# Kernel tuning notes

Hardware: AMD Instinct MI355X
Metric: run time of the kernel (lower is better)

The kernel has to match this reference:

```python
import jax, jax.numpy as jnp
import numpy as np

C = 256
RED = 8
DQK = C // RED  # 32


def setup_inputs() -> dict:
    key = jax.random.key(0)
    ks = jax.random.split(key, 8)
    B, H, W = 8, 64, 64
    x = jax.random.normal(ks[0], (B, C, H, W), dtype=jnp.float32)
    # 1x1 conv weights stored as [out, in]; biases [out]
    Wq = jax.random.normal(ks[1], (DQK, C), dtype=jnp.float32) * 0.02
    bq = jax.random.normal(ks[2], (DQK,), dtype=jnp.float32) * 0.02
    Wk = jax.random.normal(ks[3], (DQK, C), dtype=jnp.float32) * 0.02
    bk = jax.random.normal(ks[4], (DQK,), dtype=jnp.float32) * 0.02
    Wv = jax.random.normal(ks[5], (C, C), dtype=jnp.float32) * 0.02
    bv = jax.random.normal(ks[6], (C,), dtype=jnp.float32) * 0.02
    gamma = jax.random.normal(ks[7], (1,), dtype=jnp.float32) * 0.1
    return {"x": x, "Wq": Wq, "bq": bq, "Wk": Wk, "bk": bk, "Wv": Wv, "bv": bv, "gamma": gamma}


def reference(x, Wq, bq, Wk, bk, Wv, bv, gamma):
    B, Cc, H, W = x.shape
    N = H * W
    xf = x.reshape(B, Cc, N)                       # (B, C, N)
    # 1x1 convs == per-pixel dense projections
    q = jnp.einsum('dc,bcn->bdn', Wq, xf) + bq[None, :, None]   # (B, d, N)
    k = jnp.einsum('dc,bcn->bdn', Wk, xf) + bk[None, :, None]   # (B, d, N)
    v = jnp.einsum('ec,bcn->ben', Wv, xf) + bv[None, :, None]   # (B, C, N)
    # energy[b,i,j] = q[b,:,i] . k[b,:,j]; softmax over j (no scaling, SAGAN-style)
    energy = jnp.einsum('bdi,bdj->bij', q, k)      # (B, N, N)
    attn = jax.nn.softmax(energy, axis=-1)
    # out[b,c,i] = sum_j v[b,c,j] * attn[b,i,j]
    out = jnp.einsum('bcj,bij->bci', v, attn)      # (B, C, N)
    out = out.reshape(B, Cc, H, W)
    return gamma[0] * out + x
```

## Files before the change

kernel.cpp:

```cpp
#include <hip/hip_runtime.h>

#define NB 8
#define CCH 256
#define DQK 32
#define NPIX 4096

typedef __attribute__((ext_vector_type(8))) short short8;
typedef __attribute__((ext_vector_type(4))) float f32x4;
typedef __attribute__((ext_vector_type(4))) unsigned short ushort4v;

static __device__ __forceinline__ unsigned short f2bf(float f) {
  unsigned int u = __builtin_bit_cast(unsigned int, f);
  u += 0x7FFFu + ((u >> 16) & 1u);
  return (unsigned short)(u >> 16);
}
static __device__ __forceinline__ unsigned int pack2bf(float a, float b) {
  return (unsigned int)f2bf(a) | ((unsigned int)f2bf(b) << 16);
}

__global__ __launch_bounds__(256) void wconv_kernel(
    const float* __restrict__ Wq, const float* __restrict__ Wk,
    const float* __restrict__ Wv, unsigned short* __restrict__ Wbf) {
  const int e = (blockIdx.x * 256 + threadIdx.x) * 4;
  const int m = e >> 8, c = e & 255;
  const float* src;
  if (m < 32) src = Wq + (size_t)m * CCH;
  else if (m < 64) src = Wk + (size_t)(m - 32) * CCH;
  else src = Wv + (size_t)(m - 64) * CCH;
  const float4 v = *(const float4*)(src + c);
  ushort4v o;
  o[0] = f2bf(v.x); o[1] = f2bf(v.y); o[2] = f2bf(v.z); o[3] = f2bf(v.w);
  *(ushort4v*)(Wbf + e) = o;
}

__global__ __launch_bounds__(256) void xt_kernel(
    const float* __restrict__ x, unsigned short* __restrict__ xT) {
  const int t = threadIdx.x;
  const int b = blockIdx.x & 7;
  const int p = (blockIdx.x >> 3) * 64 + (t & 63);
  const int w = t >> 6;
  const float* xb = x + (size_t)b * CCH * NPIX + p;
  unsigned short* dst = xT + ((size_t)b * NPIX + p) * CCH + 64 * w;
#pragma unroll
  for (int g = 0; g < 8; ++g) {
    short8 o;
#pragma unroll
    for (int j = 0; j < 8; ++j)
      o[j] = (short)f2bf(xb[(size_t)(64 * w + 8 * g + j) * NPIX]);
    *(short8*)(dst + 8 * g) = o;
  }
}

__global__ __launch_bounds__(256) void proj_kernel(
    const unsigned short* __restrict__ xT, const unsigned short* __restrict__ Wbf,
    const float* __restrict__ bq, const float* __restrict__ bk,
    const float* __restrict__ bv,
    unsigned short* __restrict__ Qb, unsigned short* __restrict__ Kb,
    unsigned short* __restrict__ Vb) {
  const int t = threadIdx.x;
  const int b = blockIdx.x & 7;
  const int i0 = (blockIdx.x >> 3) * 64;
  const int w = t >> 6, l = t & 63;
  const int lc = l & 15, lg = l >> 4;
  const int m0w = 80 * w;
  const unsigned short* xrow = xT + ((size_t)b * NPIX + i0 + lc) * CCH + lg * 8;
  const unsigned short* wrow = Wbf + (size_t)(m0w + lc) * CCH + lg * 8;

  f32x4 acc[5][4];
#pragma unroll
  for (int mt = 0; mt < 5; ++mt)
#pragma unroll
    for (int nt = 0; nt < 4; ++nt) acc[mt][nt] = (f32x4){0.f, 0.f, 0.f, 0.f};

#pragma unroll
  for (int kk = 0; kk < 8; ++kk) {
    short8 af[5];
#pragma unroll
    for (int mt = 0; mt < 5; ++mt)
      af[mt] = *(const short8*)(wrow + (size_t)(mt * 16) * CCH + kk * 32);
    short8 bf[4];
#pragma unroll
    for (int nt = 0; nt < 4; ++nt)
      bf[nt] = *(const short8*)(xrow + (size_t)(nt * 16) * CCH + kk * 32);
#pragma unroll
    for (int nt = 0; nt < 4; ++nt)
#pragma unroll
      for (int mt = 0; mt < 5; ++mt)
        acc[mt][nt] = __builtin_amdgcn_mfma_f32_16x16x32_bf16(af[mt], bf[nt], acc[mt][nt], 0, 0, 0);
  }
#pragma unroll
  for (int mt = 0; mt < 5; ++mt) {
    const int mbase = m0w + mt * 16;
    const int mrow = mbase + 4 * lg;
    if (mbase < 64) {
      const bool isQ = (mbase < 32);
      const float scale = isQ ? 1.44269504f : 1.0f;
      const float* bias = isQ ? (bq + mrow) : (bk + (mrow - 32));
      unsigned short* dst = isQ ? (Qb + (size_t)b * NPIX * DQK + mrow)
                                : (Kb + (size_t)b * NPIX * DQK + (mrow - 32));
      const float b0 = bias[0], b1 = bias[1], b2 = bias[2], b3 = bias[3];
#pragma unroll
      for (int nt = 0; nt < 4; ++nt) {
        const int i = i0 + nt * 16 + lc;
        ushort4v o;
        o[0] = f2bf((acc[mt][nt][0] + b0) * scale);
        o[1] = f2bf((acc[mt][nt][1] + b1) * scale);
        o[2] = f2bf((acc[mt][nt][2] + b2) * scale);
        o[3] = f2bf((acc[mt][nt][3] + b3) * scale);
        *(ushort4v*)(dst + (size_t)i * DQK) = o;
      }
    } else {
      const int vrow = mbase - 64 + 4 * lg;
#pragma unroll
      for (int jj = 0; jj < 4; ++jj) {
        const float bias = bv[vrow + jj];
        unsigned short* vdst = Vb + ((size_t)b * CCH + vrow + jj) * NPIX + i0;
#pragma unroll
        for (int nt = 0; nt < 4; ++nt)
          vdst[nt * 16 + lc] = f2bf(acc[mt][nt][jj] + bias);
      }
    }
  }
}

union AttnSmem {
  unsigned short p[2][64 * 64];
  float tsc[4][16 * 68];
};

__global__ __launch_bounds__(256, 2) void attn_kernel(
    const unsigned short* __restrict__ Qb,
    const unsigned short* __restrict__ Kb,
    const unsigned short* __restrict__ Vb,
    const float* __restrict__ x,
    const float* __restrict__ gammap,
    float* __restrict__ out) {
  __shared__ AttnSmem sm;
  __shared__ float l_lds[64];
  const int t = threadIdx.x;
  const int w = t >> 6, l = t & 63;
  const int lc = l & 15, lg = l >> 4;
  const int b = blockIdx.x & 7;
  const int q0 = (blockIdx.x >> 3) * 64;

  const unsigned short* Kl = Kb + (size_t)b * NPIX * DQK + (size_t)lc * DQK + lg * 8;
  const unsigned short* Vl = Vb + ((size_t)b * CCH + 64 * w + lc) * NPIX + lg * 8;
  const short8 qa = *(const short8*)(Qb + (size_t)b * NPIX * DQK +
                                     (size_t)(q0 + 16 * w + lc) * DQK + lg * 8);
  const f32x4 zero4 = {0.f, 0.f, 0.f, 0.f};
  const int pwb = (16 * w + lc) * 128;
  const int psw = (lc & 7) << 3;

  f32x4 acc[4][4];
#pragma unroll
  for (int mt = 0; mt < 4; ++mt)
#pragma unroll
    for (int ct = 0; ct < 4; ++ct) acc[mt][ct] = (f32x4){0.f, 0.f, 0.f, 0.f};
  float psum = 0.f;

  short8 vfA[8], vfB[8], kfA[4], kfB[4];

#pragma unroll
  for (int kt = 0; kt < 4; ++kt)
    kfA[kt] = *(const short8*)(Kl + (size_t)(kt * 16) * DQK);
#pragma unroll
  for (int kt = 0; kt < 4; ++kt) {
    const f32x4 s = __builtin_amdgcn_mfma_f32_16x16x32_bf16(kfA[kt], qa, zero4, 0, 0, 0);
    const float p0 = __builtin_exp2f(s[0]), p1 = __builtin_exp2f(s[1]);
    const float p2 = __builtin_exp2f(s[2]), p3 = __builtin_exp2f(s[3]);
    psum += (p0 + p1) + (p2 + p3);
    uint2 wv; wv.x = pack2bf(p0, p1); wv.y = pack2bf(p2, p3);
    *(uint2*)((char*)sm.p[0] + pwb + (((16 * kt + 4 * lg) ^ psw) << 1)) = wv;
  }
#pragma unroll
  for (int ct = 0; ct < 4; ++ct) {
    vfA[ct] = *(const short8*)(Vl + (size_t)(16 * ct) * NPIX);
    vfA[4 + ct] = *(const short8*)(Vl + (size_t)(16 * ct) * NPIX + 32);
  }
#pragma unroll
  for (int kt = 0; kt < 4; ++kt)
    kfB[kt] = *(const short8*)(Kl + (size_t)(64 + kt * 16) * DQK);
  __syncthreads();

#define ATTN_ITER(T, BUF, VF, KF_CUR, VF_NXT, KF_NXT)                               \
  {                                                                                 \
    const int t_ = (T);                                                             \
    if (t_ < 63) {      \
      const size_t kb2 = (size_t)(t_ + 1) * 64;                                     \
      _Pragma("unroll") for (int ct = 0; ct < 4; ++ct) {                            \
        VF_NXT[ct] = *(const short8*)(Vl + (size_t)(16 * ct) * NPIX + kb2);         \
        VF_NXT[4 + ct] = *(const short8*)(Vl + (size_t)(16 * ct) * NPIX + kb2 + 32);\
      }                                                                             \
      if (t_ < 62) {                                                                \
        const size_t kk2 = (size_t)(t_ + 2) * 64;                                   \
        _Pragma("unroll") for (int kt = 0; kt < 4; ++kt)                            \
          KF_NXT[kt] = *(const short8*)(Kl + (kk2 + kt * 16) * DQK);                \
      }                                                                             \
    }                                                                               \
    unsigned short* pb_ = sm.p[BUF];                                                \
    unsigned short* pb2_ = sm.p[(BUF) ^ 1];                                         \
    _Pragma("unroll") for (int ks2 = 0; ks2 < 2; ++ks2) {                           \
      short8 pa[4];                                                                 \
      _Pragma("unroll") for (int mt = 0; mt < 4; ++mt)                              \
        pa[mt] = *(const short8*)((const char*)pb_ + (16 * mt + lc) * 128 +         \
                                  (((32 * ks2 + 8 * lg) ^ psw) << 1));              \
      _Pragma("unroll") for (int ct = 0; ct < 4; ++ct)                              \
        _Pragma("unroll") for (int mt = 0; mt < 4; ++mt)                            \
          acc[mt][ct] = __builtin_amdgcn_mfma_f32_16x16x32_bf16(                    \
              pa[mt], VF[ks2 * 4 + ct], acc[mt][ct], 0, 0, 0);                      \
    }                                                                               \
    if (t_ < 63) {                                                                  \
      _Pragma("unroll") for (int kt = 0; kt < 4; ++kt) {                            \
        const f32x4 s = __builtin_amdgcn_mfma_f32_16x16x32_bf16(                    \
            KF_CUR[kt], qa, zero4, 0, 0, 0);                                        \
        const float p0 = __builtin_exp2f(s[0]), p1 = __builtin_exp2f(s[1]);         \
        const float p2 = __builtin_exp2f(s[2]), p3 = __builtin_exp2f(s[3]);         \
        psum += (p0 + p1) + (p2 + p3);                                              \
        uint2 wv; wv.x = pack2bf(p0, p1); wv.y = pack2bf(p2, p3);                   \
        *(uint2*)((char*)pb2_ + pwb + (((16 * kt + 4 * lg) ^ psw) << 1)) = wv;      \
      }                                                                             \
    }                                                                               \
    asm volatile("s_waitcnt lgkmcnt(0)\n\ts_barrier" ::: "memory");                 \
  }

  for (int ks = 0; ks < 64; ks += 2) {
    ATTN_ITER(ks, 0, vfA, kfB, vfB, kfA);
    ATTN_ITER(ks + 1, 1, vfB, kfA, vfA, kfB);
  }
#undef ATTN_ITER

  {
    float v = psum;
    v += __shfl_xor(v, 16);
    v += __shfl_xor(v, 32);
    if (l < 16) l_lds[16 * w + lc] = v;
  }
  __syncthreads();

  const float g = gammap[0];
  float linv4[4][4];
#pragma unroll
  for (int mt = 0; mt < 4; ++mt)
#pragma unroll
    for (int jj = 0; jj < 4; ++jj)
      linv4[mt][jj] = g / l_lds[16 * mt + 4 * lg + jj];

  float* tw = sm.tsc[w];
  const float* xbp = x + (size_t)b * CCH * NPIX;
  float* ob = out + (size_t)b * CCH * NPIX;
#pragma unroll
  for (int ct = 0; ct < 4; ++ct) {
#pragma unroll
    for (int mt = 0; mt < 4; ++mt) {
      f32x4 o;
#pragma unroll
      for (int jj = 0; jj < 4; ++jj) o[jj] = acc[mt][ct][jj] * linv4[mt][jj];
      *(f32x4*)(tw + lc * 68 + 16 * mt + 4 * lg) = o;
    }
#pragma unroll
    for (int r = 0; r < 4; ++r) {
      const int crow = 4 * r + lg;
      const f32x4 o = *(const f32x4*)(tw + crow * 68 + lc * 4);
      const size_t idx = (size_t)(64 * w + 16 * ct + crow) * NPIX + (size_t)(q0 + lc * 4);
      const float4 xv = *(const float4*)(xbp + idx);
      float4 ov;
      ov.x = o[0] + xv.x; ov.y = o[1] + xv.y; ov.z = o[2] + xv.z; ov.w = o[3] + xv.w;
      *(float4*)(ob + idx) = ov;
    }
  }
}

extern "C" void kernel_launch(void* const* d_in, const int* in_sizes, int n_in,
                              void* d_out, int out_size, void* d_ws, size_t ws_size,
                              hipStream_t stream) {
  (void)in_sizes; (void)n_in; (void)out_size; (void)ws_size;
  const float* x     = (const float*)d_in[0];
  const float* Wq    = (const float*)d_in[1];
  const float* bq    = (const float*)d_in[2];
  const float* Wk    = (const float*)d_in[3];
  const float* bk    = (const float*)d_in[4];
  const float* Wv    = (const float*)d_in[5];
  const float* bv    = (const float*)d_in[6];
  const float* gamma = (const float*)d_in[7];

  unsigned short* Wbf = (unsigned short*)d_ws;
  unsigned short* Qb  = Wbf + 320 * CCH;
  unsigned short* Kb  = Qb + (size_t)NB * NPIX * DQK;
  unsigned short* Vb  = Kb + (size_t)NB * NPIX * DQK;
  unsigned short* xT  = (unsigned short*)d_out;

  wconv_kernel<<<80, 256, 0, stream>>>(Wq, Wk, Wv, Wbf);
  xt_kernel<<<512, 256, 0, stream>>>(x, xT);
  proj_kernel<<<512, 256, 0, stream>>>(xT, Wbf, bq, bk, bv, Qb, Kb, Vb);
  attn_kernel<<<512, 256, 0, stream>>>(Qb, Kb, Vb, x, gamma, (float*)d_out);
}
```

Measured before the change: 289.0 us.

## Keep softmax probabilities in registers and split channels across eight waves

The attention kernel is restructured so each of eight waves owns 32 value channels and recomputes the full 64-query score tile itself. Exponentiated scores are packed to bf16 with a truncating byte-permute and fed straight into the PV MFMA as A operands, which removes the LDS round trip and the per-step barrier. The exp2 prescale folded into Q is replaced by __expf. The cost is that every wave redundantly computes QK^T (eight times more score MFMAs and exps), V is no longer register-prefetched, and bf16 rounding becomes truncation.

New measurement: 540.3 us. +87.0%, slower.

```diff
diff --git a/kernel.cpp b/kernel.cpp
--- a/kernel.cpp
+++ b/kernel.cpp
@@ -7,6 +7,7 @@
 
 typedef __attribute__((ext_vector_type(8))) short short8;
 typedef __attribute__((ext_vector_type(4))) float f32x4;
+typedef __attribute__((ext_vector_type(4))) unsigned int uint4v;
 typedef __attribute__((ext_vector_type(4))) unsigned short ushort4v;
 
 static __device__ __forceinline__ unsigned short f2bf(float f) {
@@ -14,8 +15,9 @@
   u += 0x7FFFu + ((u >> 16) & 1u);
   return (unsigned short)(u >> 16);
 }
-static __device__ __forceinline__ unsigned int pack2bf(float a, float b) {
-  return (unsigned int)f2bf(a) | ((unsigned int)f2bf(b) << 16);
+static __device__ __forceinline__ unsigned int permpack(float lo, float hi) {
+  return __builtin_amdgcn_perm(__builtin_bit_cast(unsigned int, hi),
+                               __builtin_bit_cast(unsigned int, lo), 0x07060302u);
 }
 
 __global__ __launch_bounds__(256) void wconv_kernel(
@@ -94,7 +96,6 @@
     const int mrow = mbase + 4 * lg;
     if (mbase < 64) {
       const bool isQ = (mbase < 32);
-      const float scale = isQ ? 1.44269504f : 1.0f;
       const float* bias = isQ ? (bq + mrow) : (bk + (mrow - 32));
       unsigned short* dst = isQ ? (Qb + (size_t)b * NPIX * DQK + mrow)
                                 : (Kb + (size_t)b * NPIX * DQK + (mrow - 32));
@@ -103,10 +104,10 @@
       for (int nt = 0; nt < 4; ++nt) {
         const int i = i0 + nt * 16 + lc;
         ushort4v o;
-        o[0] = f2bf((acc[mt][nt][0] + b0) * scale);
-        o[1] = f2bf((acc[mt][nt][1] + b1) * scale);
-        o[2] = f2bf((acc[mt][nt][2] + b2) * scale);
-        o[3] = f2bf((acc[mt][nt][3] + b3) * scale);
+        o[0] = f2bf(acc[mt][nt][0] + b0);
+        o[1] = f2bf(acc[mt][nt][1] + b1);
+        o[2] = f2bf(acc[mt][nt][2] + b2);
+        o[3] = f2bf(acc[mt][nt][3] + b3);
         *(ushort4v*)(dst + (size_t)i * DQK) = o;
       }
     } else {
@@ -123,148 +124,133 @@
   }
 }
 
-union AttnSmem {
-  unsigned short p[2][64 * 64];
-  float tsc[4][16 * 68];
-};
-
-__global__ __launch_bounds__(256, 2) void attn_kernel(
+__global__ __launch_bounds__(512) void attn_kernel(
     const unsigned short* __restrict__ Qb,
     const unsigned short* __restrict__ Kb,
     const unsigned short* __restrict__ Vb,
     const float* __restrict__ x,
     const float* __restrict__ gammap,
     float* __restrict__ out) {
-  __shared__ AttnSmem sm;
-  __shared__ float l_lds[64];
+  __shared__ float tsc[8][64 * 17];
   const int t = threadIdx.x;
   const int w = t >> 6, l = t & 63;
-  const int lc = l & 15, lg = l >> 4;
+  const int lc = l & 15, lg = (l >> 4) & 3;
   const int b = blockIdx.x & 7;
   const int q0 = (blockIdx.x >> 3) * 64;
+  const int c0 = 32 * w;
 
   const unsigned short* Kl = Kb + (size_t)b * NPIX * DQK + (size_t)lc * DQK + lg * 8;
-  const unsigned short* Vl = Vb + ((size_t)b * CCH + 64 * w + lc) * NPIX + lg * 8;
-  const short8 qa = *(const short8*)(Qb + (size_t)b * NPIX * DQK +
-                                     (size_t)(q0 + 16 * w + lc) * DQK + lg * 8);
+  const unsigned short* Ql = Qb + (size_t)b * NPIX * DQK + (size_t)(q0 + lc) * DQK + lg * 8;
+  const unsigned short* Vl = Vb + ((size_t)b * CCH + c0 + lc) * NPIX;
   const f32x4 zero4 = {0.f, 0.f, 0.f, 0.f};
-  const int pwb = (16 * w + lc) * 128;
-  const int psw = (lc & 7) << 3;
-
-  f32x4 acc[4][4];
-#pragma unroll
-  for (int mt = 0; mt < 4; ++mt)
-#pragma unroll
-    for (int ct = 0; ct < 4; ++ct) acc[mt][ct] = (f32x4){0.f, 0.f, 0.f, 0.f};
-  float psum = 0.f;
-
-  short8 vfA[8], vfB[8], kfA[4], kfB[4];
-
+
+  short8 qa[4];
+#pragma unroll
+  for (int qf = 0; qf < 4; ++qf)
+    qa[qf] = *(const short8*)(Ql + (size_t)(qf * 16) * DQK);
+
+  f32x4 acc[4][2];
+#pragma unroll
+  for (int qf = 0; qf < 4; ++qf)
+#pragma unroll
+    for (int ct = 0; ct < 2; ++ct) acc[qf][ct] = zero4;
+  float psum[4] = {0.f, 0.f, 0.f, 0.f};
+
+  short8 kfA[4], kfB[4];
 #pragma unroll
   for (int kt = 0; kt < 4; ++kt)
     kfA[kt] = *(const short8*)(Kl + (size_t)(kt * 16) * DQK);
-#pragma unroll
-  for (int kt = 0; kt < 4; ++kt) {
-    const f32x4 s = __builtin_amdgcn_mfma_f32_16x16x32_bf16(kfA[kt], qa, zero4, 0, 0, 0);
-    const float p0 = __builtin_exp2f(s[0]), p1 = __builtin_exp2f(s[1]);
-    const float p2 = __builtin_exp2f(s[2]), p3 = __builtin_exp2f(s[3]);
-    psum += (p0 + p1) + (p2 + p3);
-    uint2 wv; wv.x = pack2bf(p0, p1); wv.y = pack2bf(p2, p3);
-    *(uint2*)((char*)sm.p[0] + pwb + (((16 * kt + 4 * lg) ^ psw) << 1)) = wv;
-  }
-#pragma unroll
-  for (int ct = 0; ct < 4; ++ct) {
-    vfA[ct] = *(const short8*)(Vl + (size_t)(16 * ct) * NPIX);
-    vfA[4 + ct] = *(const short8*)(Vl + (size_t)(16 * ct) * NPIX + 32);
-  }
-#pragma unroll
-  for (int kt = 0; kt < 4; ++kt)
-    kfB[kt] = *(const short8*)(Kl + (size_t)(64 + kt * 16) * DQK);
-  __syncthreads();
-
-#define ATTN_ITER(T, BUF, VF, KF_CUR, VF_NXT, KF_NXT)                               \
-  {                                                                                 \
-    const int t_ = (T);                                                             \
-    if (t_ < 63) {      \
-      const size_t kb2 = (size_t)(t_ + 1) * 64;                                     \
-      _Pragma("unroll") for (int ct = 0; ct < 4; ++ct) {                            \
-        VF_NXT[ct] = *(const short8*)(Vl + (size_t)(16 * ct) * NPIX + kb2);         \
-        VF_NXT[4 + ct] = *(const short8*)(Vl + (size_t)(16 * ct) * NPIX + kb2 + 32);\
-      }                                                                             \
-      if (t_ < 62) {                                                                \
-        const size_t kk2 = (size_t)(t_ + 2) * 64;                                   \
-        _Pragma("unroll") for (int kt = 0; kt < 4; ++kt)                            \
-          KF_NXT[kt] = *(const short8*)(Kl + (kk2 + kt * 16) * DQK);                \
-      }                                                                             \
-    }                                                                               \
-    unsigned short* pb_ = sm.p[BUF];                                                \
-    unsigned short* pb2_ = sm.p[(BUF) ^ 1];                                         \
-    _Pragma("unroll") for (int ks2 = 0; ks2 < 2; ++ks2) {                           \
-      short8 pa[4];                                                                 \
-      _Pragma("unroll") for (int mt = 0; mt < 4; ++mt)                              \
-        pa[mt] = *(const short8*)((const char*)pb_ + (16 * mt + lc) * 128 +         \
-                                  (((32 * ks2 + 8 * lg) ^ psw) << 1));              \
-      _Pragma("unroll") for (int ct = 0; ct < 4; ++ct)                              \
-        _Pragma("unroll") for (int mt = 0; mt < 4; ++mt)                            \
-          acc[mt][ct] = __builtin_amdgcn_mfma_f32_16x16x32_bf16(                    \
-              pa[mt], VF[ks2 * 4 + ct], acc[mt][ct], 0, 0, 0);                      \
-    }                                                                               \
-    if (t_ < 63) {                                                                  \
-      _Pragma("unroll") for (int kt = 0; kt < 4; ++kt) {                            \
-        const f32x4 s = __builtin_amdgcn_mfma_f32_16x16x32_bf16(                    \
-            KF_CUR[kt], qa, zero4, 0, 0, 0);                                        \
-        const float p0 = __builtin_exp2f(s[0]), p1 = __builtin_exp2f(s[1]);         \
-        const float p2 = __builtin_exp2f(s[2]), p3 = __builtin_exp2f(s[3]);         \
-        psum += (p0 + p1) + (p2 + p3);                                              \
-        uint2 wv; wv.x = pack2bf(p0, p1); wv.y = pack2bf(p2, p3);                   \
-        *(uint2*)((char*)pb2_ + pwb + (((16 * kt + 4 * lg) ^ psw) << 1)) = wv;      \
-      }                                                                             \
-    }                                                                               \
-    asm volatile("s_waitcnt lgkmcnt(0)\n\ts_barrier" ::: "memory");                 \
+
+#define ATTN_STEP(T, KF_CUR, KF_NXT)                                              \
+  {                                                                               \
+    const int t_ = (T);                                                           \
+    const size_t k0 = (size_t)t_ * 64;                                            \
+             \
+    uint2 vlo[2][2], vhi[2][2];                                                   \
+    _Pragma("unroll") for (int ct = 0; ct < 2; ++ct)                              \
+      _Pragma("unroll") for (int h = 0; h < 2; ++h) {                             \
+        const unsigned short* vb_ = Vl + (size_t)(16 * ct) * NPIX + k0 + 32 * h + 4 * lg; \
+        vlo[ct][h] = *(const uint2*)vb_;                                          \
+        vhi[ct][h] = *(const uint2*)(vb_ + 16);                                   \
+      }                                                                           \
+                                                        \
+    const size_t kn = (size_t)(t_ < 63 ? t_ + 1 : 63) * 64;                       \
+    _Pragma("unroll") for (int kt = 0; kt < 4; ++kt)                              \
+      KF_NXT[kt] = *(const short8*)(Kl + (kn + kt * 16) * DQK);                   \
+                                        \
+    unsigned int pr[4][4][2];                                                     \
+    _Pragma("unroll") for (int kt = 0; kt < 4; ++kt) {                            \
+      f32x4 s[4];                                                                 \
+      _Pragma("unroll") for (int qf = 0; qf < 4; ++qf)                            \
+        s[qf] = __builtin_amdgcn_mfma_f32_16x16x32_bf16(KF_CUR[kt], qa[qf], zero4, 0, 0, 0); \
+      _Pragma("unroll") for (int qf = 0; qf < 4; ++qf) {                          \
+        const float p0 = __expf(s[qf][0]), p1 = __expf(s[qf][1]);                 \
+        const float p2 = __expf(s[qf][2]), p3 = __expf(s[qf][3]);                 \
+        psum[qf] += (p0 + p1) + (p2 + p3);                                        \
+        pr[kt][qf][0] = permpack(p0, p1);                                         \
+        pr[kt][qf][1] = permpack(p2, p3);                                         \
+      }                                                                           \
+    }                                                                             \
+      \
+    _Pragma("unroll") for (int h = 0; h < 2; ++h) {                               \
+      short8 pa[4], vf[2];                                                        \
+      _Pragma("unroll") for (int qf = 0; qf < 4; ++qf)                            \
+        pa[qf] = __builtin_bit_cast(short8, (uint4v){pr[2 * h][qf][0], pr[2 * h][qf][1], \
+                                                     pr[2 * h + 1][qf][0], pr[2 * h + 1][qf][1]}); \
+      _Pragma("unroll") for (int ct = 0; ct < 2; ++ct)                            \
+        vf[ct] = __builtin_bit_cast(short8, (uint4v){vlo[ct][h].x, vlo[ct][h].y,  \
+                                                     vhi[ct][h].x, vhi[ct][h].y}); \
+      _Pragma("unroll") for (int ct = 0; ct < 2; ++ct)                            \
+        _Pragma("unroll") for (int qf = 0; qf < 4; ++qf)                          \
+          acc[qf][ct] = __builtin_amdgcn_mfma_f32_16x16x32_bf16(pa[qf], vf[ct], acc[qf][ct], 0, 0, 0); \
+    }                                                                             \
   }
 
   for (int ks = 0; ks < 64; ks += 2) {
-    ATTN_ITER(ks, 0, vfA, kfB, vfB, kfA);
-    ATTN_ITER(ks + 1, 1, vfB, kfA, vfA, kfB);
-  }
-#undef ATTN_ITER
-
-  {
-    float v = psum;
+    ATTN_STEP(ks, kfA, kfB);
+    ATTN_STEP(ks + 1, kfB, kfA);
+  }
+#undef ATTN_STEP
+
+  float lred[4];
+#pragma unroll
+  for (int qf = 0; qf < 4; ++qf) {
+    float v = psum[qf];
     v += __shfl_xor(v, 16);
     v += __shfl_xor(v, 32);
-    if (l < 16) l_lds[16 * w + lc] = v;
-  }
-  __syncthreads();
-
+    lred[qf] = v;
+  }
   const float g = gammap[0];
-  float linv4[4][4];
-#pragma unroll
-  for (int mt = 0; mt < 4; ++mt)
+  float linv[4][4];
+#pragma unroll
+  for (int qf = 0; qf < 4; ++qf)
 #pragma unroll
     for (int jj = 0; jj < 4; ++jj)
-      linv4[mt][jj] = g / l_lds[16 * mt + 4 * lg + jj];
-
-  float* tw = sm.tsc[w];
-  const float* xbp = x + (size_t)b * CCH * NPIX;
-  float* ob = out + (size_t)b * CCH * NPIX;
-#pragma unroll
-  for (int ct = 0; ct < 4; ++ct) {
-#pragma unroll
-    for (int mt = 0; mt < 4; ++mt) {
-      f32x4 o;
-#pragma unroll
-      for (int jj = 0; jj < 4; ++jj) o[jj] = acc[mt][ct][jj] * linv4[mt][jj];
-      *(f32x4*)(tw + lc * 68 + 16 * mt + 4 * lg) = o;
-    }
-#pragma unroll
-    for (int r = 0; r < 4; ++r) {
-      const int crow = 4 * r + lg;
-      const f32x4 o = *(const f32x4*)(tw + crow * 68 + lc * 4);
-      const size_t idx = (size_t)(64 * w + 16 * ct + crow) * NPIX + (size_t)(q0 + lc * 4);
+      linv[qf][jj] = g / __shfl(lred[qf], 4 * lg + jj);
+
+  float* tw = tsc[w];
+  const float* xbp = x + ((size_t)b * CCH + c0) * NPIX;
+  float* ob = out + ((size_t)b * CCH + c0) * NPIX;
+#pragma unroll
+  for (int ct = 0; ct < 2; ++ct) {
+#pragma unroll
+    for (int qf = 0; qf < 4; ++qf)
+#pragma unroll
+      for (int jj = 0; jj < 4; ++jj)
+        tw[(16 * qf + 4 * lg + jj) * 17 + lc] = acc[qf][ct][jj] * linv[qf][jj];
+#pragma unroll
+    for (int p2 = 0; p2 < 4; ++p2) {
+      const int cl = (l >> 4) + 4 * p2;
+      const int qx = 4 * lc;
+      float4 o;
+      o.x = tw[(qx + 0) * 17 + cl];
+      o.y = tw[(qx + 1) * 17 + cl];
+      o.z = tw[(qx + 2) * 17 + cl];
+      o.w = tw[(qx + 3) * 17 + cl];
+      const size_t idx = (size_t)(16 * ct + cl) * NPIX + q0 + qx;
       const float4 xv = *(const float4*)(xbp + idx);
       float4 ov;
-      ov.x = o[0] + xv.x; ov.y = o[1] + xv.y; ov.z = o[2] + xv.z; ov.w = o[3] + xv.w;
+      ov.x = o.x + xv.x; ov.y = o.y + xv.y; ov.z = o.z + xv.z; ov.w = o.w + xv.w;
       *(float4*)(ob + idx) = ov;
     }
   }
@@ -292,5 +278,5 @@
   wconv_kernel<<<80, 256, 0, stream>>>(Wq, Wk, Wv, Wbf);
   xt_kernel<<<512, 256, 0, stream>>>(x, xT);
   proj_kernel<<<512, 256, 0, stream>>>(xT, Wbf, bq, bk, bv, Qb, Kb, Vb);
-  attn_kernel<<<512, 256, 0, stream>>>(Qb, Kb, Vb, x, gamma, (float*)d_out);
-}
+  attn_kernel<<<512, 512, 0, stream>>>(Qb, Kb, Vb, x, gamma, (float*)d_out);
+}
```

## Split attention block across 8 waves with per-wave key-tile scores and channel slices

Applied to the files above, without the earlier changes.

The attention kernel moves from 256 to 512 threads per block. Each wave now computes scores for one 16-key sub-tile across 32 queries and accumulates PV for a 32-channel slice, instead of each wave owning 16 queries and 64 channels. Row sums are reduced through a small partial-sum LDS array. The exp2 with a folded log2e scale is replaced by __expf, and bf16 packing now uses a truncating byte permute instead of round-to-nearest. The aim is more waves in flight, fewer registers per wave, and cheaper packing, at the cost of reduced precision and more LDS traffic and barrier participants.

Measured after the change: 332.0 us. 1.15x slower.

```diff
diff --git a/kernel.cpp b/kernel.cpp
--- a/kernel.cpp
+++ b/kernel.cpp
@@ -7,6 +7,7 @@
 
 typedef __attribute__((ext_vector_type(8))) short short8;
 typedef __attribute__((ext_vector_type(4))) float f32x4;
+typedef __attribute__((ext_vector_type(4))) unsigned int uint4v;
 typedef __attribute__((ext_vector_type(4))) unsigned short ushort4v;
 
 static __device__ __forceinline__ unsigned short f2bf(float f) {
@@ -14,8 +15,9 @@
   u += 0x7FFFu + ((u >> 16) & 1u);
   return (unsigned short)(u >> 16);
 }
-static __device__ __forceinline__ unsigned int pack2bf(float a, float b) {
-  return (unsigned int)f2bf(a) | ((unsigned int)f2bf(b) << 16);
+static __device__ __forceinline__ unsigned int permpack(float lo, float hi) {
+  return __builtin_amdgcn_perm(__builtin_bit_cast(unsigned int, hi),
+                               __builtin_bit_cast(unsigned int, lo), 0x07060302u);
 }
 
 __global__ __launch_bounds__(256) void wconv_kernel(
@@ -94,7 +96,6 @@
     const int mrow = mbase + 4 * lg;
     if (mbase < 64) {
       const bool isQ = (mbase < 32);
-      const float scale = isQ ? 1.44269504f : 1.0f;
       const float* bias = isQ ? (bq + mrow) : (bk + (mrow - 32));
       unsigned short* dst = isQ ? (Qb + (size_t)b * NPIX * DQK + mrow)
                                 : (Kb + (size_t)b * NPIX * DQK + (mrow - 32));
@@ -103,10 +104,10 @@
       for (int nt = 0; nt < 4; ++nt) {
         const int i = i0 + nt * 16 + lc;
         ushort4v o;
-        o[0] = f2bf((acc[mt][nt][0] + b0) * scale);
-        o[1] = f2bf((acc[mt][nt][1] + b1) * scale);
-        o[2] = f2bf((acc[mt][nt][2] + b2) * scale);
-        o[3] = f2bf((acc[mt][nt][3] + b3) * scale);
+        o[0] = f2bf(acc[mt][nt][0] + b0);
+        o[1] = f2bf(acc[mt][nt][1] + b1);
+        o[2] = f2bf(acc[mt][nt][2] + b2);
+        o[3] = f2bf(acc[mt][nt][3] + b3);
         *(ushort4v*)(dst + (size_t)i * DQK) = o;
       }
     } else {
@@ -125,10 +126,10 @@
 
 union AttnSmem {
   unsigned short p[2][64 * 64];
-  float tsc[4][16 * 68];
+  float tsc[8][16 * 68];
 };
 
-__global__ __launch_bounds__(256, 2) void attn_kernel(
+__global__ __launch_bounds__(512, 4) void attn_kernel(
     const unsigned short* __restrict__ Qb,
     const unsigned short* __restrict__ Kb,
     const unsigned short* __restrict__ Vb,
@@ -136,88 +137,91 @@
     const float* __restrict__ gammap,
     float* __restrict__ out) {
   __shared__ AttnSmem sm;
-  __shared__ float l_lds[64];
+  __shared__ float lpart[64 * 4];
   const int t = threadIdx.x;
   const int w = t >> 6, l = t & 63;
   const int lc = l & 15, lg = l >> 4;
+  const int ktw = w & 3, qh = w >> 2;
   const int b = blockIdx.x & 7;
   const int q0 = (blockIdx.x >> 3) * 64;
-
-  const unsigned short* Kl = Kb + (size_t)b * NPIX * DQK + (size_t)lc * DQK + lg * 8;
-  const unsigned short* Vl = Vb + ((size_t)b * CCH + 64 * w + lc) * NPIX + lg * 8;
-  const short8 qa = *(const short8*)(Qb + (size_t)b * NPIX * DQK +
-                                     (size_t)(q0 + 16 * w + lc) * DQK + lg * 8);
+  const int c0 = 32 * w;
+  const int psw = (lc & 7) << 3;
+
+  const unsigned short* Kl = Kb + (size_t)b * NPIX * DQK + (size_t)(16 * ktw + lc) * DQK + lg * 8;
+  const unsigned short* Ql = Qb + (size_t)b * NPIX * DQK + (size_t)(q0 + 32 * qh + lc) * DQK + lg * 8;
+  const unsigned short* Vl = Vb + ((size_t)b * CCH + c0 + lc) * NPIX + lg * 8;
   const f32x4 zero4 = {0.f, 0.f, 0.f, 0.f};
-  const int pwb = (16 * w + lc) * 128;
-  const int psw = (lc & 7) << 3;
-
-  f32x4 acc[4][4];
-#pragma unroll
-  for (int mt = 0; mt < 4; ++mt)
-#pragma unroll
-    for (int ct = 0; ct < 4; ++ct) acc[mt][ct] = (f32x4){0.f, 0.f, 0.f, 0.f};
-  float psum = 0.f;
-
-  short8 vfA[8], vfB[8], kfA[4], kfB[4];
-
-#pragma unroll
-  for (int kt = 0; kt < 4; ++kt)
-    kfA[kt] = *(const short8*)(Kl + (size_t)(kt * 16) * DQK);
-#pragma unroll
-  for (int kt = 0; kt < 4; ++kt) {
-    const f32x4 s = __builtin_amdgcn_mfma_f32_16x16x32_bf16(kfA[kt], qa, zero4, 0, 0, 0);
-    const float p0 = __builtin_exp2f(s[0]), p1 = __builtin_exp2f(s[1]);
-    const float p2 = __builtin_exp2f(s[2]), p3 = __builtin_exp2f(s[3]);
-    psum += (p0 + p1) + (p2 + p3);
-    uint2 wv; wv.x = pack2bf(p0, p1); wv.y = pack2bf(p2, p3);
-    *(uint2*)((char*)sm.p[0] + pwb + (((16 * kt + 4 * lg) ^ psw) << 1)) = wv;
-  }
-#pragma unroll
-  for (int ct = 0; ct < 4; ++ct) {
-    vfA[ct] = *(const short8*)(Vl + (size_t)(16 * ct) * NPIX);
-    vfA[4 + ct] = *(const short8*)(Vl + (size_t)(16 * ct) * NPIX + 32);
-  }
-#pragma unroll
-  for (int kt = 0; kt < 4; ++kt)
-    kfB[kt] = *(const short8*)(Kl + (size_t)(64 + kt * 16) * DQK);
+
+  short8 qa[2];
+#pragma unroll
+  for (int f = 0; f < 2; ++f)
+    qa[f] = *(const short8*)(Ql + (size_t)(16 * f) * DQK);
+
+  f32x4 acc[4][2];
+#pragma unroll
+  for (int qf = 0; qf < 4; ++qf)
+#pragma unroll
+    for (int cf = 0; cf < 2; ++cf) acc[qf][cf] = zero4;
+  float psum[2] = {0.f, 0.f};
+
+  short8 vfA[4], vfB[4], kfA, kfB;
+  kfA = *(const short8*)Kl;
+
+#pragma unroll
+  for (int f = 0; f < 2; ++f) {
+    const f32x4 s = __builtin_amdgcn_mfma_f32_16x16x32_bf16(kfA, qa[f], zero4, 0, 0, 0);
+    const float p0 = __expf(s[0]), p1 = __expf(s[1]);
+    const float p2 = __expf(s[2]), p3 = __expf(s[3]);
+    psum[f] += (p0 + p1) + (p2 + p3);
+    uint2 wv; wv.x = permpack(p0, p1); wv.y = permpack(p2, p3);
+    *(uint2*)((char*)sm.p[0] + (32 * qh + 16 * f + lc) * 128 +
+              (((16 * ktw + 4 * lg) ^ psw) << 1)) = wv;
+  }
+#pragma unroll
+  for (int ks = 0; ks < 2; ++ks)
+#pragma unroll
+    for (int cf = 0; cf < 2; ++cf)
+      vfA[ks * 2 + cf] = *(const short8*)(Vl + (size_t)(16 * cf) * NPIX + 32 * ks);
+  kfB = *(const short8*)(Kl + (size_t)64 * DQK);
   __syncthreads();
 
 #define ATTN_ITER(T, BUF, VF, KF_CUR, VF_NXT, KF_NXT)                               \
   {                                                                                 \
     const int t_ = (T);                                                             \
-    if (t_ < 63) {      \
+    if (t_ < 63) {                                     \
       const size_t kb2 = (size_t)(t_ + 1) * 64;                                     \
-      _Pragma("unroll") for (int ct = 0; ct < 4; ++ct) {                            \
-        VF_NXT[ct] = *(const short8*)(Vl + (size_t)(16 * ct) * NPIX + kb2);         \
-        VF_NXT[4 + ct] = *(const short8*)(Vl + (size_t)(16 * ct) * NPIX + kb2 + 32);\
-      }                                                                             \
-      if (t_ < 62) {                                                                \
-        const size_t kk2 = (size_t)(t_ + 2) * 64;                                   \
-        _Pragma("unroll") for (int kt = 0; kt < 4; ++kt)                            \
-          KF_NXT[kt] = *(const short8*)(Kl + (kk2 + kt * 16) * DQK);                \
-      }                                                                             \
+      _Pragma("unroll") for (int ks = 0; ks < 2; ++ks)                              \
+        _Pragma("unroll") for (int cf = 0; cf < 2; ++cf)                            \
+          VF_NXT[ks * 2 + cf] =                                                     \
+              *(const short8*)(Vl + (size_t)(16 * cf) * NPIX + kb2 + 32 * ks);      \
+      if (t_ < 62)                                                                  \
+        KF_NXT = *(const short8*)(Kl + (size_t)(t_ + 2) * 64 * DQK);                \
     }                                                                               \
-    unsigned short* pb_ = sm.p[BUF];                                                \
-    unsigned short* pb2_ = sm.p[(BUF) ^ 1];                                         \
-    _Pragma("unroll") for (int ks2 = 0; ks2 < 2; ++ks2) {                           \
+    f32x4 s_[2];                                                                    \
+    if (t_ < 63) {                 \
+      _Pragma("unroll") for (int f = 0; f < 2; ++f)                                 \
+        s_[f] = __builtin_amdgcn_mfma_f32_16x16x32_bf16(KF_CUR, qa[f], zero4, 0, 0, 0); \
+    }                                                                               \
+    const char* pb_ = (const char*)sm.p[BUF];                                       \
+    char* pb2_ = (char*)sm.p[(BUF) ^ 1];                                            \
+    _Pragma("unroll") for (int ks = 0; ks < 2; ++ks) {                              \
       short8 pa[4];                                                                 \
-      _Pragma("unroll") for (int mt = 0; mt < 4; ++mt)                              \
-        pa[mt] = *(const short8*)((const char*)pb_ + (16 * mt + lc) * 128 +         \
-                                  (((32 * ks2 + 8 * lg) ^ psw) << 1));              \
-      _Pragma("unroll") for (int ct = 0; ct < 4; ++ct)                              \
-        _Pragma("unroll") for (int mt = 0; mt < 4; ++mt)                            \
-          acc[mt][ct] = __builtin_amdgcn_mfma_f32_16x16x32_bf16(                    \
-              pa[mt], VF[ks2 * 4 + ct], acc[mt][ct], 0, 0, 0);                      \
+      _Pragma("unroll") for (int qf = 0; qf < 4; ++qf)                              \
+        pa[qf] = *(const short8*)(pb_ + (16 * qf + lc) * 128 +                      \
+                                  (((32 * ks + 8 * lg) ^ psw) << 1));               \
+      _Pragma("unroll") for (int cf = 0; cf < 2; ++cf)                              \
+        _Pragma("unroll") for (int qf = 0; qf < 4; ++qf)                            \
+          acc[qf][cf] = __builtin_amdgcn_mfma_f32_16x16x32_bf16(                    \
+              pa[qf], VF[ks * 2 + cf], acc[qf][cf], 0, 0, 0);                       \
     }                                                                               \
-    if (t_ < 63) {                                                                  \
-      _Pragma("unroll") for (int kt = 0; kt < 4; ++kt) {                            \
-        const f32x4 s = __builtin_amdgcn_mfma_f32_16x16x32_bf16(                    \
-            KF_CUR[kt], qa, zero4, 0, 0, 0);                                        \
-        const float p0 = __builtin_exp2f(s[0]), p1 = __builtin_exp2f(s[1]);         \
-        const float p2 = __builtin_exp2f(s[2]), p3 = __builtin_exp2f(s[3]);         \
-        psum += (p0 + p1) + (p2 + p3);                                              \
-        uint2 wv; wv.x = pack2bf(p0, p1); wv.y = pack2bf(p2, p3);                   \
-        *(uint2*)((char*)pb2_ + pwb + (((16 * kt + 4 * lg) ^ psw) << 1)) = wv;      \
+    if (t_ < 63) {                                 \
+      _Pragma("unroll") for (int f = 0; f < 2; ++f) {                               \
+        const float p0 = __expf(s_[f][0]), p1 = __expf(s_[f][1]);                   \
+        const float p2 = __expf(s_[f][2]), p3 = __expf(s_[f][3]);                   \
+        psum[f] += (p0 + p1) + (p2 + p3);                                           \
+        uint2 wv; wv.x = permpack(p0, p1); wv.y = permpack(p2, p3);                 \
+        *(uint2*)(pb2_ + (32 * qh + 16 * f + lc) * 128 +                            \
+                  (((16 * ktw + 4 * lg) ^ psw) << 1)) = wv;                         \
       }                                                                             \
     }                                                                               \
     asm volatile("s_waitcnt lgkmcnt(0)\n\ts_barrier" ::: "memory");                 \
@@ -229,39 +233,43 @@
   }
 #undef ATTN_ITER
 
-  {
-    float v = psum;
+#pragma unroll
+  for (int f = 0; f < 2; ++f) {
+    float v = psum[f];
     v += __shfl_xor(v, 16);
     v += __shfl_xor(v, 32);
-    if (l < 16) l_lds[16 * w + lc] = v;
+    if (l < 16) lpart[(32 * qh + 16 * f + lc) * 4 + ktw] = v;
   }
   __syncthreads();
 
   const float g = gammap[0];
-  float linv4[4][4];
-#pragma unroll
-  for (int mt = 0; mt < 4; ++mt)
-#pragma unroll
-    for (int jj = 0; jj < 4; ++jj)
-      linv4[mt][jj] = g / l_lds[16 * mt + 4 * lg + jj];
+  float linv[4][4];
+#pragma unroll
+  for (int qf = 0; qf < 4; ++qf)
+#pragma unroll
+    for (int jj = 0; jj < 4; ++jj) {
+      const f32x4 lp = *(const f32x4*)&lpart[(16 * qf + 4 * lg + jj) * 4];
+      linv[qf][jj] = g / ((lp[0] + lp[1]) + (lp[2] + lp[3]));
+    }
 
   float* tw = sm.tsc[w];
-  const float* xbp = x + (size_t)b * CCH * NPIX;
-  float* ob = out + (size_t)b * CCH * NPIX;
-#pragma unroll
-  for (int ct = 0; ct < 4; ++ct) {
-#pragma unroll
-    for (int mt = 0; mt < 4; ++mt) {
+  const float* xbp = x + ((size_t)b * CCH + c0) * NPIX;
+  float* ob = out + ((size_t)b * CCH + c0) * NPIX;
+#pragma unroll
+  for (int cf = 0; cf < 2; ++cf) {
+#pragma unroll
+    for (int qf = 0; qf < 4; ++qf) {
       f32x4 o;
 #pragma unroll
-      for (int jj = 0; jj < 4; ++jj) o[jj] = acc[mt][ct][jj] * linv4[mt][jj];
-      *(f32x4*)(tw + lc * 68 + 16 * mt + 4 * lg) = o;
+      for (int jj = 0; jj < 4; ++jj) o[jj] = acc[qf][cf][jj] * linv[qf][jj];
+      *(f32x4*)(tw + lc * 68 + 16 * qf + 4 * lg) = o;
     }
 #pragma unroll
-    for (int r = 0; r < 4; ++r) {
-      const int crow = 4 * r + lg;
-      const f32x4 o = *(const f32x4*)(tw + crow * 68 + lc * 4);
-      const size_t idx = (size_t)(64 * w + 16 * ct + crow) * NPIX + (size_t)(q0 + lc * 4);
+    for (int p2 = 0; p2 < 4; ++p2) {
+      const int cl = lg + 4 * p2;
+      const int qx = 4 * lc;
+      const f32x4 o = *(const f32x4*)(tw + cl * 68 + qx);
+      const size_t idx = (size_t)(16 * cf + cl) * NPIX + q0 + qx;
       const float4 xv = *(const float4*)(xbp + idx);
       float4 ov;
       ov.x = o[0] + xv.x; ov.y = o[1] + xv.y; ov.z = o[2] + xv.z; ov.w = o[3] + xv.w;
@@ -292,5 +300,5 @@
   wconv_kernel<<<80, 256, 0, stream>>>(Wq, Wk, Wv, Wbf);
   xt_kernel<<<512, 256, 0, stream>>>(x, xT);
   proj_kernel<<<512, 256, 0, stream>>>(xT, Wbf, bq, bk, bv, Qb, Kb, Vb);
-  attn_kernel<<<512, 256, 0, stream>>>(Qb, Kb, Vb, x, gamma, (float*)d_out);
-}
+  attn_kernel<<<512, 512, 0, stream>>>(Qb, Kb, Vb, x, gamma, (float*)d_out);
+}
```
